# Performance work log

Measured on AMD Instinct MI355X. Metric: run time of the kernel, lower is better.

## Reference

```python
import jax, jax.numpy as jnp
import numpy as np
import math

B, S, F, D = 8, 2048, 1024, 1024
NEG = -1e9


def setup_inputs() -> dict:
    key = jax.random.key(0)
    ks = jax.random.split(key, 5)
    x = jax.random.normal(ks[0], (B, S, F), dtype=jnp.float32)
    r_mat = jax.random.normal(ks[1], (B, S, S), dtype=jnp.float32)
    # shared causal attention mask [S, S] (1 = keep, 0 = masked)
    attn_mask = jnp.tril(jnp.ones((S, S), dtype=jnp.float32))
    # per-batch padding mask [B, 1, S]: last 128 tokens of half the batch padded
    pad = jnp.ones((B, 1, S), dtype=jnp.float32)
    pad = pad.at[B // 2:, :, S - 128:].set(0.0)
    Wq = jax.random.normal(ks[2], (F, D), dtype=jnp.float32) / math.sqrt(F)
    Wk = jax.random.normal(ks[3], (F, D), dtype=jnp.float32) / math.sqrt(F)
    Wv = jax.random.normal(ks[4], (F, D), dtype=jnp.float32) / math.sqrt(F)
    return {"x": x, "r_mat": r_mat, "attn_mask": attn_mask, "pad_mask": pad,
            "Wq": Wq, "Wk": Wk, "Wv": Wv}


def reference(x, r_mat, attn_mask, pad_mask, Wq, Wk, Wv):
    scale = math.sqrt(x.shape[-1])  # original scales by sqrt(features)
    q = jnp.einsum('bsf,fd->bsd', x, Wq)
    k = jnp.einsum('bsf,fd->bsd', x, Wk)
    v = jnp.einsum('bsf,fd->bsd', x, Wv)
    scores = jnp.einsum('bsd,btd->bst', q, k) / scale  # [B, S, S]
    keep = (pad_mask != 0.0) & (attn_mask[None] != 0.0)  # [B, S, S] broadcast
    r = jnp.where(keep, r_mat, NEG)
    r = jax.nn.softmax(r, axis=-1)
    scores = jnp.where(keep, scores + r, NEG)
    prob = jax.nn.softmax(scores, axis=-1)
    return jnp.einsum('bst,btd->bsd', prob, v)
```

## Files before the change

kernel.cpp:

```cpp
#include <hip/hip_runtime.h>
#include <hip/hip_bf16.h>

#define B_ 8
#define S_ 2048
#define F_ 1024
#define D_ 1024

typedef unsigned short u16;
typedef float f32x4 __attribute__((ext_vector_type(4)));
typedef __bf16 bf16x8 __attribute__((ext_vector_type(8)));
typedef unsigned short u16x8 __attribute__((ext_vector_type(8)));

__device__ __forceinline__ u16 f2bf(float f) {
  union { float f; unsigned u; } v; v.f = f;
  unsigned r = v.u + 0x7fff + ((v.u >> 16) & 1);
  return (u16)(r >> 16);
}
__device__ __forceinline__ float bf2f(u16 b) {
  union { unsigned u; float f; } v; v.u = ((unsigned)b) << 16;
  return v.f;
}

__device__ __forceinline__ void stage16(const u16* g, u16* l) {
  __builtin_amdgcn_global_load_lds(
      (const __attribute__((address_space(1))) void*)g,
      (__attribute__((address_space(3))) void*)l, 16, 0, 0);
}


__global__ void cast_x(const float* __restrict__ x, u16* __restrict__ xb, int n4) {
  int i = blockIdx.x * blockDim.x + threadIdx.x;
  int stride = gridDim.x * blockDim.x;
  for (; i < n4; i += stride) {
    float4 v = ((const float4*)x)[i];
    ushort4 o;
    o.x = f2bf(v.x); o.y = f2bf(v.y); o.z = f2bf(v.z); o.w = f2bf(v.w);
    ((ushort4*)xb)[i] = o;
  }
}

__global__ void transW(const float* __restrict__ Wq, const float* __restrict__ Wk,
                       const float* __restrict__ Wv, u16* __restrict__ Wt) {
  __shared__ float tile[32][33];
  int z = blockIdx.z;
  const float* W = (z == 0) ? Wq : ((z == 1) ? Wk : Wv);
  int f0 = blockIdx.y * 32, d0 = blockIdx.x * 32;
  int tx = threadIdx.x & 31, ty = threadIdx.x >> 5;
  for (int i = 0; i < 4; i++)
    tile[ty + i * 8][tx] = W[(size_t)(f0 + ty + i * 8) * D_ + d0 + tx];
  __syncthreads();
  u16* o = Wt + (size_t)z * D_ * F_;
  for (int i = 0; i < 4; i++)
    o[(size_t)(d0 + ty + i * 8) * F_ + f0 + tx] = f2bf(tile[tx][ty + i * 8]);
}

__global__ __launch_bounds__(256) void r_rowsum(const float* __restrict__ r,
                                                const float* __restrict__ pm,
                                                float* __restrict__ rs) {
  int row = blockIdx.x;
  int b = row >> 11, s = row & 2047;
  const float4* rp = (const float4*)(r + (size_t)row * S_);
  const float4* pp = (const float4*)(pm + (size_t)b * S_);
  int nv = (s >> 2) + 1;
  float acc = 0.f;
  for (int i = threadIdx.x; i < nv; i += 256) {
    float4 rv = rp[i];
    float4 pv = pp[i];
    int t0 = i << 2;
    #pragma unroll
    for (int j = 0; j < 4; j++) {
      int t = t0 + j;
      if (t <= s && (&pv.x)[j] != 0.f) acc += __expf((&rv.x)[j] - 16.f);
    }
  }
  for (int off = 1; off < 64; off <<= 1) acc += __shfl_xor(acc, off);
  __shared__ float wsum[4];
  int lane = threadIdx.x & 63, w = threadIdx.x >> 6;
  if (lane == 0) wsum[w] = acc;
  __syncthreads();
  if (threadIdx.x == 0) rs[row] = wsum[0] + wsum[1] + wsum[2] + wsum[3];
}

__global__ __launch_bounds__(256) void er_pass(const float* __restrict__ r,
                                               const float* __restrict__ pm,
                                               const float* __restrict__ rs_r,
                                               u16* __restrict__ Er) {
  int row = blockIdx.x * 2 + (threadIdx.x >> 7);
  int b = row >> 11, s = row & 2047;
  int rowlim = ((s >> 8) + 1) << 8;
  float invr = 1.f / rs_r[row];
  const float4* rp = (const float4*)(r + (size_t)row * S_);
  const float4* pp = (const float4*)(pm + (size_t)b * S_);
  ushort4* erow = (ushort4*)(Er + (size_t)row * S_);
  int tc = threadIdx.x & 127;
  for (int c4 = tc; c4 * 4 < rowlim; c4 += 128) {
    float4 rv = rp[c4];
    float4 pv = pp[c4];
    int t0 = c4 * 4;
    ushort4 o;
    #pragma unroll
    for (int j = 0; j < 4; j++) {
      bool keep = (t0 + j <= s) && ((&pv.x)[j] != 0.f);
      float e = keep ? __expf(__expf((&rv.x)[j] - 16.f) * invr) : 0.f;
      (&o.x)[j] = f2bf(e);
    }
    erow[c4] = o;
  }
}


__device__ __forceinline__ void stageA(const u16* __restrict__ src, int ld, int h,
                                       u16* ldsA, int w, int l) {
  int base = ((w >> 2) * 128) + h * 64 + ((w & 3) * 16);
  int r = l >> 3, ch = (l & 7) ^ (l >> 3);
  #pragma unroll
  for (int i = 0; i < 2; i++) {
    int row = base + i * 8;
    stage16(src + (size_t)(row + r) * ld + ch * 8, ldsA + row * 64);
  }
}
__device__ __forceinline__ void stageB(const u16* __restrict__ src, int ld, int h,
                                       u16* ldsB, int w, int l) {
  int base = h * 128 + w * 16;
  int r = l >> 3, ch = (l & 7) ^ (l >> 3);
  #pragma unroll
  for (int i = 0; i < 2; i++) {
    int row = base + i * 8;
    stage16(src + (size_t)(row + r) * ld + ch * 8, ldsB + row * 64);
  }
}

__device__ __forceinline__ bf16x8 readfrag(const u16* lds, int row, int ks, int hi) {
  int c = ((ks << 6) + (hi << 4)) ^ ((row & 7) << 4);
  return *(const bf16x8*)((const char*)lds + row * 128 + c);
}

#define MFMA_QUAD(MB, KS)                                                        \
  __builtin_amdgcn_s_setprio(1);                                                 \
  _Pragma("unroll")                                                              \
  for (int m = 0; m < 4; m++)                                                    \
    _Pragma("unroll")                                                            \
    for (int n = 0; n < 4; n++)                                                  \
      acc[(MB) + m][n] = __builtin_amdgcn_mfma_f32_16x16x32_bf16(                \
          af[m], bfr[(KS)*4 + n], acc[(MB) + m][n], 0, 0, 0);                    \
  __builtin_amdgcn_s_setprio(0);

__device__ __forceinline__ void gemm256(const u16* __restrict__ A, int lda,
                                        const u16* __restrict__ B, int ldb,
                                        int nT, u16* lds, f32x4 acc[8][4]) {
  const int t = threadIdx.x, w = t >> 6, l = t & 63;
  const int wr = w >> 2, wc = w & 3;
  u16* A0 = lds;           u16* B0 = lds + 16384;
  u16* A1 = lds + 32768;   u16* B1 = lds + 49152;

  #pragma unroll
  for (int m = 0; m < 8; m++)
    #pragma unroll
    for (int n = 0; n < 4; n++)
      #pragma unroll
      for (int j = 0; j < 4; j++) acc[m][n][j] = 0.f;

  stageB(B, ldb, 0, B0, w, l);
  stageB(B, ldb, 1, B0, w, l);
  stageA(A, lda, 0, A0, w, l);
  stageA(A, lda, 1, A0, w, l);
  if (nT > 1) stageA(A + 64, lda, 0, A1, w, l);
  asm volatile("s_waitcnt vmcnt(4)" ::: "memory");
  __builtin_amdgcn_sched_barrier(0);
  __builtin_amdgcn_s_barrier();

  for (int kt = 0; kt < nT; kt++) {
    u16* cA = (kt & 1) ? A1 : A0;
    u16* cB = (kt & 1) ? B1 : B0;
    u16* nA = (kt & 1) ? A0 : A1;
    u16* nB = (kt & 1) ? B0 : B1;
    const u16* An1 = A + (size_t)(kt + 1) * 64;
    const u16* Bn1 = B + (size_t)(kt + 1) * 64;
    const u16* An2 = A + (size_t)(kt + 2) * 64;
    const bool has1 = (kt + 1 < nT), has2 = (kt + 2 < nT);
    const int arow = wr * 128 + (l & 15), brow = wc * 64 + (l & 15), hi = l >> 4;
    bf16x8 af[4], bfr[8];

    #pragma unroll
    for (int m = 0; m < 4; m++) af[m] = readfrag(cA, arow + m * 16, 0, hi);
    #pragma unroll
    for (int n = 0; n < 4; n++) bfr[n] = readfrag(cB, brow + n * 16, 0, hi);
    if (has1) stageB(Bn1, ldb, 0, nB, w, l);
    __builtin_amdgcn_s_barrier();
    MFMA_QUAD(0, 0)
    __builtin_amdgcn_s_barrier();

    #pragma unroll
    for (int m = 0; m < 4; m++) af[m] = readfrag(cA, arow + m * 16, 1, hi);
    #pragma unroll
    for (int n = 0; n < 4; n++) bfr[4 + n] = readfrag(cB, brow + n * 16, 1, hi);
    if (has1) {
      stageB(Bn1, ldb, 1, nB, w, l);
      asm volatile("s_waitcnt vmcnt(4)" ::: "memory");
    } else {
      asm volatile("s_waitcnt vmcnt(0)" ::: "memory");
    }
    __builtin_amdgcn_sched_barrier(0);
    __builtin_amdgcn_s_barrier();
    MFMA_QUAD(0, 1)
    __builtin_amdgcn_s_barrier();

    #pragma unroll
    for (int m = 0; m < 4; m++) af[m] = readfrag(cA, arow + 64 + m * 16, 0, hi);
    if (has2) stageA(An2, lda, 0, cA, w, l);
    __builtin_amdgcn_s_barrier();
    MFMA_QUAD(4, 0)
    __builtin_amdgcn_s_barrier();

    #pragma unroll
    for (int m = 0; m < 4; m++) af[m] = readfrag(cA, arow + 64 + m * 16, 1, hi);
    if (has1) stageA(An1, lda, 1, nA, w, l);
    if (has1 && has2)  { asm volatile("s_waitcnt vmcnt(4)" ::: "memory"); }
    else if (has1)     { asm volatile("s_waitcnt vmcnt(2)" ::: "memory"); }
    __builtin_amdgcn_sched_barrier(0);
    __builtin_amdgcn_s_barrier();
    MFMA_QUAD(4, 1)
    __builtin_amdgcn_s_barrier();
  }
}

__device__ __forceinline__ void store256_bf16(f32x4 acc[8][4], u16* smem,
                                              u16* dst, int ld) {
  int t = threadIdx.x, w = t >> 6, l = t & 63;
  int wr = w >> 2, wc = w & 3;
  #pragma unroll
  for (int q = 0; q < 4; q++) {
    __syncthreads();
    if (wr == (q >> 1)) {
      int mb = (q & 1) * 4;
      #pragma unroll
      for (int mm = 0; mm < 4; mm++)
        #pragma unroll
        for (int j = 0; j < 4; j++) {
          int row = mm * 16 + (l >> 4) * 4 + j;
          #pragma unroll
          for (int n = 0; n < 4; n++)
            smem[row * 264 + wc * 64 + n * 16 + (l & 15)] = f2bf(acc[mb + mm][n][j]);
        }
    }
    __syncthreads();
    #pragma unroll
    for (int i = 0; i < 4; i++) {
      int idx = i * 512 + t;
      int row = idx >> 5, ch = idx & 31;
      *(u16x8*)(dst + (size_t)(q * 64 + row) * ld + ch * 8) =
          *(const u16x8*)(smem + row * 264 + ch * 8);
    }
  }
}

__global__ __launch_bounds__(512, 2) void gemm_qkv(
    const u16* __restrict__ xb, const u16* __restrict__ Wt,
    u16* __restrict__ qb, u16* __restrict__ kb, u16* __restrict__ vT) {
  __shared__ __align__(16) u16 lds[65536];
  int z = blockIdx.z;
  f32x4 acc[8][4];
  if (z < 2) {
    int m0 = blockIdx.x * 256, n0 = blockIdx.y * 256;
    gemm256(xb + (size_t)m0 * F_, F_,
            Wt + (size_t)z * D_ * F_ + (size_t)n0 * F_, F_, F_ / 64, lds, acc);
    store256_bf16(acc, lds, ((z == 0) ? qb : kb) + (size_t)m0 * D_ + n0, D_);
  } else {
    int d0 = blockIdx.y * 256, s0g = blockIdx.x * 256;
    gemm256(Wt + 2ULL * D_ * F_ + (size_t)d0 * F_, F_,
            xb + (size_t)s0g * F_, F_, F_ / 64, lds, acc);
    int b = s0g >> 11, s0 = s0g & 2047;
    store256_bf16(acc, lds, vT + (size_t)b * D_ * S_ + (size_t)d0 * S_ + s0, S_);
  }
}

__global__ __launch_bounds__(512, 2) void attn_scores(
    const u16* __restrict__ qb, const u16* __restrict__ kb,
    u16* __restrict__ P, float* __restrict__ rowsum) {
  int mt = blockIdx.x, nt = blockIdx.y, b = blockIdx.z;
  if (nt > mt) return;
  __shared__ __align__(16) u16 lds[65536];
  int m0 = mt * 256, n0 = nt * 256;
  f32x4 acc[8][4];
  gemm256(qb + ((size_t)b * S_ + m0) * D_, D_,
          kb + ((size_t)b * S_ + n0) * D_, D_, D_ / 64, lds, acc);
  int t = threadIdx.x, w = t >> 6, l = t & 63;
  int wr = w >> 2, wc = w & 3;
  float* fs = (float*)lds;
  #pragma unroll
  for (int q = 0; q < 4; q++) {
    __syncthreads();
    if (wr == (q >> 1)) {
      int mb = (q & 1) * 4;
      #pragma unroll
      for (int mm = 0; mm < 4; mm++)
        #pragma unroll
        for (int j = 0; j < 4; j++) {
          int row = mm * 16 + (l >> 4) * 4 + j;
          #pragma unroll
          for (int n = 0; n < 4; n++)
            fs[row * 260 + wc * 64 + n * 16 + (l & 15)] = acc[mb + mm][n][j];
        }
    }
    __syncthreads();
    int row = t >> 3, cg = t & 7;
    int srow = m0 + q * 64 + row;
    u16* prow = P + (size_t)b * S_ * S_ + (size_t)srow * S_ + n0 + cg * 32;
    const float* fsc = fs + row * 260 + cg * 32;
    float rsum = 0.f;
    #pragma unroll
    for (int cc = 0; cc < 4; cc++) {
      int ch = (cg + cc) & 3;
      u16x8 er = *(const u16x8*)(prow + ch * 8);
      u16x8 o;
      #pragma unroll
      for (int k = 0; k < 8; k++) {
        float e = __expf(fmaf(fsc[ch * 8 + k], 0.03125f, -16.f)) * bf2f(er[k]);
        u16 pb = f2bf(e); o[k] = pb; rsum += bf2f(pb);
      }
      *(u16x8*)(prow + ch * 8) = o;
    }
    for (int off = 1; off < 8; off <<= 1) rsum += __shfl_xor(rsum, off);
    if ((t & 7) == 0) atomicAdd(&rowsum[b * S_ + srow], rsum);
  }
}

__global__ __launch_bounds__(512, 2) void attn_pv(
    const u16* __restrict__ P, const u16* __restrict__ vT,
    const float* __restrict__ rowsum, float* __restrict__ out) {
  __shared__ __align__(16) u16 lds[65536];
  int mt = blockIdx.x, dt = blockIdx.y, b = blockIdx.z;
  int m0 = mt * 256, n0 = dt * 256;
  int kmax = m0 + 256;
  f32x4 acc[8][4];
  gemm256(P + ((size_t)b * S_ + m0) * S_, S_,
          vT + ((size_t)b * D_ + n0) * S_, S_, kmax / 64, lds, acc);
  int t = threadIdx.x, w = t >> 6, l = t & 63;
  int wr = w >> 2, wc = w & 3;
  float* fs = (float*)lds;
  #pragma unroll
  for (int q = 0; q < 4; q++) {
    __syncthreads();
    if (wr == (q >> 1)) {
      int mb = (q & 1) * 4;
      #pragma unroll
      for (int mm = 0; mm < 4; mm++)
        #pragma unroll
        for (int j = 0; j < 4; j++) {
          int row = mm * 16 + (l >> 4) * 4 + j;
          float inv = 1.f / rowsum[b * S_ + m0 + q * 64 + row];
          #pragma unroll
          for (int n = 0; n < 4; n++)
            fs[row * 260 + wc * 64 + n * 16 + (l & 15)] = acc[mb + mm][n][j] * inv;
        }
    }
    __syncthreads();
    #pragma unroll
    for (int i = 0; i < 8; i++) {
      int idx = i * 512 + t;
      int row = idx >> 6, c4 = (idx & 63) << 2;
      *(float4*)(out + ((size_t)b * S_ + m0 + q * 64 + row) * D_ + n0 + c4) =
          *(const float4*)(fs + row * 260 + c4);
    }
  }
}

extern "C" void kernel_launch(void* const* d_in, const int* in_sizes, int n_in,
                              void* d_out, int out_size, void* d_ws, size_t ws_size,
                              hipStream_t stream) {
  const float* x     = (const float*)d_in[0];
  const float* r_mat = (const float*)d_in[1];
  const float* pm    = (const float*)d_in[3];
  const float* Wq    = (const float*)d_in[4];
  const float* Wk    = (const float*)d_in[5];
  const float* Wv    = (const float*)d_in[6];
  float* out = (float*)d_out;
  char* ws = (char*)d_ws;

  u16*   qb     = (u16*)(ws + 0);
  u16*   kb     = (u16*)(ws + 33554432ULL);
  u16*   vT     = (u16*)(ws + 67108864ULL);
  float* rs_r   = (float*)(ws + 100663296ULL);
  float* rowsum = (float*)(ws + 100728832ULL);
  u16*   P      = (u16*)(ws + 100794368ULL);
  u16*   xb     = (u16*)(ws + 100794368ULL);
  u16*   Wt     = (u16*)(ws + 134348800ULL);

  cast_x<<<dim3(2048), dim3(256), 0, stream>>>(x, xb, (B_ * S_ * F_) / 4);
  transW<<<dim3(32, 32, 3), dim3(256), 0, stream>>>(Wq, Wk, Wv, Wt);
  r_rowsum<<<dim3(B_ * S_), dim3(256), 0, stream>>>(r_mat, pm, rs_r);
  gemm_qkv<<<dim3(64, 4, 3), dim3(512), 0, stream>>>(xb, Wt, qb, kb, vT);
  hipMemsetAsync(rowsum, 0, B_ * S_ * sizeof(float), stream);
  er_pass<<<dim3(B_ * S_ / 2), dim3(256), 0, stream>>>(r_mat, pm, rs_r, P);
  attn_scores<<<dim3(8, 8, 8), dim3(512), 0, stream>>>(qb, kb, P, rowsum);
  attn_pv<<<dim3(8, 4, 8), dim3(512), 0, stream>>>(P, vT, rowsum, out);
}
```

Before: 315.2 us.

## Fuse r-softmax exponent pass into attention score epilogue and cut GEMM barriers

Removes the separate er_pass kernel and computes the masked exp of the softmaxed r matrix directly in the attn_scores epilogue, reading r_mat and the pad mask in fp32. This avoids writing and re-reading an intermediate bf16 P buffer. The GEMM main loop also drops half of its s_barrier pairs and merges the rest into sched_barrier-fenced sync points. The cost is more fp32 global traffic and exp work inside the score kernel, plus a risk of LDS hazards from the reduced barrier set.

```diff
diff --git a/kernel.cpp b/kernel.cpp
--- a/kernel.cpp
+++ b/kernel.cpp
@@ -81,33 +81,6 @@
   if (threadIdx.x == 0) rs[row] = wsum[0] + wsum[1] + wsum[2] + wsum[3];
 }
 
-__global__ __launch_bounds__(256) void er_pass(const float* __restrict__ r,
-                                               const float* __restrict__ pm,
-                                               const float* __restrict__ rs_r,
-                                               u16* __restrict__ Er) {
-  int row = blockIdx.x * 2 + (threadIdx.x >> 7);
-  int b = row >> 11, s = row & 2047;
-  int rowlim = ((s >> 8) + 1) << 8;
-  float invr = 1.f / rs_r[row];
-  const float4* rp = (const float4*)(r + (size_t)row * S_);
-  const float4* pp = (const float4*)(pm + (size_t)b * S_);
-  ushort4* erow = (ushort4*)(Er + (size_t)row * S_);
-  int tc = threadIdx.x & 127;
-  for (int c4 = tc; c4 * 4 < rowlim; c4 += 128) {
-    float4 rv = rp[c4];
-    float4 pv = pp[c4];
-    int t0 = c4 * 4;
-    ushort4 o;
-    #pragma unroll
-    for (int j = 0; j < 4; j++) {
-      bool keep = (t0 + j <= s) && ((&pv.x)[j] != 0.f);
-      float e = keep ? __expf(__expf((&rv.x)[j] - 16.f) * invr) : 0.f;
-      (&o.x)[j] = f2bf(e);
-    }
-    erow[c4] = o;
-  }
-}
-
 
 __device__ __forceinline__ void stageA(const u16* __restrict__ src, int ld, int h,
                                        u16* ldsA, int w, int l) {
@@ -135,15 +108,20 @@
   return *(const bf16x8*)((const char*)lds + row * 128 + c);
 }
 
-#define MFMA_QUAD(MB, KS)                                                        \
+#define MFMA_QUAD(MB, KB)                                                        \
   __builtin_amdgcn_s_setprio(1);                                                 \
   _Pragma("unroll")                                                              \
   for (int m = 0; m < 4; m++)                                                    \
     _Pragma("unroll")                                                            \
     for (int n = 0; n < 4; n++)                                                  \
       acc[(MB) + m][n] = __builtin_amdgcn_mfma_f32_16x16x32_bf16(                \
-          af[m], bfr[(KS)*4 + n], acc[(MB) + m][n], 0, 0, 0);                    \
+          af[m], bfr[(KB) + n], acc[(MB) + m][n], 0, 0, 0);                      \
   __builtin_amdgcn_s_setprio(0);
+
+#define SYNC_POINT()                                                             \
+  __builtin_amdgcn_sched_barrier(0);                                             \
+  __builtin_amdgcn_s_barrier();                                                  \
+  __builtin_amdgcn_sched_barrier(0);
 
 __device__ __forceinline__ void gemm256(const u16* __restrict__ A, int lda,
                                         const u16* __restrict__ B, int ldb,
@@ -166,8 +144,9 @@
   stageA(A, lda, 1, A0, w, l);
   if (nT > 1) stageA(A + 64, lda, 0, A1, w, l);
   asm volatile("s_waitcnt vmcnt(4)" ::: "memory");
-  __builtin_amdgcn_sched_barrier(0);
-  __builtin_amdgcn_s_barrier();
+  SYNC_POINT()
+
+  const int arow = wr * 128 + (l & 15), brow = wc * 64 + (l & 15), hi = l >> 4;
 
   for (int kt = 0; kt < nT; kt++) {
     u16* cA = (kt & 1) ? A1 : A0;
@@ -178,7 +157,6 @@
     const u16* Bn1 = B + (size_t)(kt + 1) * 64;
     const u16* An2 = A + (size_t)(kt + 2) * 64;
     const bool has1 = (kt + 1 < nT), has2 = (kt + 2 < nT);
-    const int arow = wr * 128 + (l & 15), brow = wc * 64 + (l & 15), hi = l >> 4;
     bf16x8 af[4], bfr[8];
 
     #pragma unroll
@@ -186,9 +164,7 @@
     #pragma unroll
     for (int n = 0; n < 4; n++) bfr[n] = readfrag(cB, brow + n * 16, 0, hi);
     if (has1) stageB(Bn1, ldb, 0, nB, w, l);
-    __builtin_amdgcn_s_barrier();
     MFMA_QUAD(0, 0)
-    __builtin_amdgcn_s_barrier();
 
     #pragma unroll
     for (int m = 0; m < 4; m++) af[m] = readfrag(cA, arow + m * 16, 1, hi);
@@ -200,27 +176,22 @@
     } else {
       asm volatile("s_waitcnt vmcnt(0)" ::: "memory");
     }
-    __builtin_amdgcn_sched_barrier(0);
-    __builtin_amdgcn_s_barrier();
-    MFMA_QUAD(0, 1)
-    __builtin_amdgcn_s_barrier();
+    SYNC_POINT()
+    MFMA_QUAD(0, 4)
 
     #pragma unroll
     for (int m = 0; m < 4; m++) af[m] = readfrag(cA, arow + 64 + m * 16, 0, hi);
     if (has2) stageA(An2, lda, 0, cA, w, l);
-    __builtin_amdgcn_s_barrier();
     MFMA_QUAD(4, 0)
-    __builtin_amdgcn_s_barrier();
 
     #pragma unroll
     for (int m = 0; m < 4; m++) af[m] = readfrag(cA, arow + 64 + m * 16, 1, hi);
     if (has1) stageA(An1, lda, 1, nA, w, l);
     if (has1 && has2)  { asm volatile("s_waitcnt vmcnt(4)" ::: "memory"); }
     else if (has1)     { asm volatile("s_waitcnt vmcnt(2)" ::: "memory"); }
-    __builtin_amdgcn_sched_barrier(0);
-    __builtin_amdgcn_s_barrier();
-    MFMA_QUAD(4, 1)
-    __builtin_amdgcn_s_barrier();
+    else               { asm volatile("s_waitcnt vmcnt(0)" ::: "memory"); }
+    SYNC_POINT()
+    MFMA_QUAD(4, 4)
   }
 }
 
@@ -276,7 +247,9 @@
 
 __global__ __launch_bounds__(512, 2) void attn_scores(
     const u16* __restrict__ qb, const u16* __restrict__ kb,
-    u16* __restrict__ P, float* __restrict__ rowsum) {
+    const float* __restrict__ r_mat, const float* __restrict__ pm,
+    const float* __restrict__ rs_r, u16* __restrict__ P,
+    float* __restrict__ rowsum) {
   int mt = blockIdx.x, nt = blockIdx.y, b = blockIdx.z;
   if (nt > mt) return;
   __shared__ __align__(16) u16 lds[65536];
@@ -287,6 +260,8 @@
   int t = threadIdx.x, w = t >> 6, l = t & 63;
   int wr = w >> 2, wc = w & 3;
   float* fs = (float*)lds;
+  const float* rb = r_mat + (size_t)b * S_ * S_;
+  const float* pmp = pm + (size_t)b * S_ + n0;
   #pragma unroll
   for (int q = 0; q < 4; q++) {
     __syncthreads();
@@ -305,17 +280,30 @@
     __syncthreads();
     int row = t >> 3, cg = t & 7;
     int srow = m0 + q * 64 + row;
+    float invr = 1.f / rs_r[b * S_ + srow];
+    const float* rrow = rb + (size_t)srow * S_ + n0 + cg * 32;
     u16* prow = P + (size_t)b * S_ * S_ + (size_t)srow * S_ + n0 + cg * 32;
     const float* fsc = fs + row * 260 + cg * 32;
     float rsum = 0.f;
     #pragma unroll
     for (int cc = 0; cc < 4; cc++) {
       int ch = (cg + cc) & 3;
-      u16x8 er = *(const u16x8*)(prow + ch * 8);
+      f32x4 q0 = *(const f32x4*)(fsc + ch * 8);
+      f32x4 q1 = *(const f32x4*)(fsc + ch * 8 + 4);
+      f32x4 r0 = *(const f32x4*)(rrow + ch * 8);
+      f32x4 r1 = *(const f32x4*)(rrow + ch * 8 + 4);
+      f32x4 p0 = *(const f32x4*)(pmp + cg * 32 + ch * 8);
+      f32x4 p1 = *(const f32x4*)(pmp + cg * 32 + ch * 8 + 4);
       u16x8 o;
       #pragma unroll
       for (int k = 0; k < 8; k++) {
-        float e = __expf(fmaf(fsc[ch * 8 + k], 0.03125f, -16.f)) * bf2f(er[k]);
+        int tc = n0 + cg * 32 + ch * 8 + k;
+        float rv = (k < 4) ? r0[k] : r1[k - 4];
+        float pmv = (k < 4) ? p0[k] : p1[k - 4];
+        float qk = (k < 4) ? q0[k] : q1[k - 4];
+        bool keep = (tc <= srow) && (pmv != 0.f);
+        float rsm = __expf(rv - 16.f) * invr;
+        float e = keep ? __expf(fmaf(qk, 0.03125f, rsm - 16.f)) : 0.f;
         u16 pb = f2bf(e); o[k] = pb; rsum += bf2f(pb);
       }
       *(u16x8*)(prow + ch * 8) = o;
@@ -391,7 +379,6 @@
   r_rowsum<<<dim3(B_ * S_), dim3(256), 0, stream>>>(r_mat, pm, rs_r);
   gemm_qkv<<<dim3(64, 4, 3), dim3(512), 0, stream>>>(xb, Wt, qb, kb, vT);
   hipMemsetAsync(rowsum, 0, B_ * S_ * sizeof(float), stream);
-  er_pass<<<dim3(B_ * S_ / 2), dim3(256), 0, stream>>>(r_mat, pm, rs_r, P);
-  attn_scores<<<dim3(8, 8, 8), dim3(512), 0, stream>>>(qb, kb, P, rowsum);
+  attn_scores<<<dim3(8, 8, 8), dim3(512), 0, stream>>>(qb, kb, r_mat, pm, rs_r, P, rowsum);
   attn_pv<<<dim3(8, 4, 8), dim3(512), 0, stream>>>(P, vT, rowsum, out);
 }
```

After: 306.7 us. 2.7% less time.
